# Performance work log

Hardware: AMD Instinct MI355X
Metric: run time of the kernel (lower is better)

Reference implementation:

```python
import jax, jax.numpy as jnp
import numpy as np
import math

HEAD_DIM = 128
DEPTH = 12
LAMBDA_INIT = 0.8 - 0.6 * math.exp(-0.3 * DEPTH)
EPS = 1e-5


def setup_inputs() -> dict:
    key = jax.random.key(0)
    ks = jax.random.split(key, 7)
    B, S, H2, D = 2, 2048, 16, HEAD_DIM  # H2 = 2 * num_diff_heads
    q = jax.random.normal(ks[0], (B, S, H2, D), dtype=jnp.float32)
    k = jax.random.normal(ks[1], (B, S, H2, D), dtype=jnp.float32)
    v = jax.random.normal(ks[2], (B, S, H2, D), dtype=jnp.float32)
    lambda_q1 = 0.1 * jax.random.normal(ks[3], (D,), dtype=jnp.float32)
    lambda_k1 = 0.1 * jax.random.normal(ks[4], (D,), dtype=jnp.float32)
    lambda_q2 = 0.1 * jax.random.normal(ks[5], (D,), dtype=jnp.float32)
    lambda_k2 = 0.1 * jax.random.normal(ks[6], (D,), dtype=jnp.float32)
    return {"q": q, "k": k, "v": v, "lambda_q1": lambda_q1, "lambda_k1": lambda_k1,
            "lambda_q2": lambda_q2, "lambda_k2": lambda_k2}


def _attn(qh, kh, v12, scale, causal_bias):
    # qh,kh: [B,S,H,D]; v12: [B,S,H,2D] (concat of v1,v2 -> same softmax shared,
    # identical math to the two separate flash calls attnX1/attnX2 concatenated)
    scores = jnp.einsum('bshd,bthd->bhst', qh, kh) * scale + causal_bias
    p = jax.nn.softmax(scores, axis=-1)
    return jnp.einsum('bhst,bthd->bshd', p, v12)  # [B,S,H,2D]


def reference(q, k, v, lambda_q1, lambda_k1, lambda_q2, lambda_k2):
    B, S, H2, D = q.shape
    H = H2 // 2
    scale = 1.0 / math.sqrt(D)
    # split_heads: '(H two) D' -> pairs of adjacent heads
    def split(x):
        x = x.reshape(B, S, H, 2, D)
        return x[..., 0, :], x[..., 1, :]
    q1, q2 = split(q)
    k1, k2 = split(k)
    v1, v2 = split(v)
    v12 = jnp.concatenate([v1, v2], axis=-1)  # [B,S,H,2D]

    causal_bias = jnp.where(jnp.tril(jnp.ones((S, S), dtype=bool)), 0.0,
                            jnp.float32(-jnp.inf))  # [S,S]

    attn1 = _attn(q1, k1, v12, scale, causal_bias)  # = cat(attn11, attn12)
    attn2 = _attn(q2, k2, v12, scale, causal_bias)  # = cat(attn21, attn22)

    lambda_1 = jnp.exp(jnp.sum(lambda_q1 * lambda_k1))
    lambda_2 = jnp.exp(jnp.sum(lambda_q2 * lambda_k2))
    lambda_full = lambda_1 - lambda_2 + LAMBDA_INIT

    attn = attn1 - lambda_full * attn2  # [B,S,H,2D]
    # RMSNorm over last dim (2D), no affine
    attn = attn * jax.lax.rsqrt(jnp.mean(attn * attn, axis=-1, keepdims=True) + EPS)
    attn = attn * (1.0 - LAMBDA_INIT)
    # '... H (two D) -> ... (H two) D'
    return attn.reshape(B, S, H, 2, D).reshape(B, S, H2, D)
```

## Files before the change

kernel.cpp:

```cpp
#include <hip/hip_runtime.h>
#include <math.h>


#define S_LEN 2048
#define ROWSTR 2048
#define NEG_BIG (-3.0e38f)
#define QSCALE (1.44269504088896f * 0.0883883476483184f)
#define SM_SHIFT 20.0f
#define LAMBDA_INIT 0.783605766532f

typedef __attribute__((ext_vector_type(8))) short short8;
typedef __attribute__((ext_vector_type(4))) float f32x4;

__device__ __forceinline__ short f2bf(float f) {
    unsigned u = __builtin_bit_cast(unsigned, f);
    u += 0x7fffu + ((u >> 16) & 1u);
    return (short)(u >> 16);
}

__device__ __forceinline__ void async16(const short* g, short* l) {
    __builtin_amdgcn_global_load_lds(
        (const __attribute__((address_space(1))) unsigned int*)g,
        (__attribute__((address_space(3))) unsigned int*)l, 16, 0, 0);
}

__global__ __launch_bounds__(256)
void prep_kernel(const float* __restrict__ k, const float* __restrict__ v,
                 short* __restrict__ kws, short* __restrict__ vws) {
    __shared__ short sT[32][258];
    const int tid = threadIdx.x;
    const int bh  = blockIdx.x >> 6;
    const int t   = blockIdx.x & 63;
    const int b   = bh >> 3;
    const int h   = bh & 7;

    {
        const int attn = tid >> 7;
        const int key  = (tid >> 2) & 31;
        const int tt   = tid & 3;
        const int s    = t * 32 + key;
        const float* src = k + (((size_t)(b * S_LEN + s) * 16) + 2 * h + attn) * 128 + tt * 32;
        short* kdst = kws + (((size_t)(bh * 64 + t)) << 13) + attn * 4096 + key * 128;
        #pragma unroll
        for (int i = 0; i < 4; ++i) {
            const int c = tt * 4 + i;
            float4 a0 = *(const float4*)(src + i * 8);
            float4 a1 = *(const float4*)(src + i * 8 + 4);
            short8 sv;
            sv[0]=f2bf(a0.x); sv[1]=f2bf(a0.y); sv[2]=f2bf(a0.z); sv[3]=f2bf(a0.w);
            sv[4]=f2bf(a1.x); sv[5]=f2bf(a1.y); sv[6]=f2bf(a1.z); sv[7]=f2bf(a1.w);
            *(short8*)(kdst + ((c ^ (key & 7)) << 3)) = sv;
        }
    }

    {
        const int key  = tid >> 3;
        const int part = tid & 7;
        const float* vsrc = v + (((size_t)(b * S_LEN + t * 32 + key) * 16) + 2 * h) * 128 + part * 32;
        #pragma unroll
        for (int i = 0; i < 4; ++i) {
            float4 a0 = *(const float4*)(vsrc + i * 8);
            float4 a1 = *(const float4*)(vsrc + i * 8 + 4);
            short8 sv;
            sv[0]=f2bf(a0.x); sv[1]=f2bf(a0.y); sv[2]=f2bf(a0.z); sv[3]=f2bf(a0.w);
            sv[4]=f2bf(a1.x); sv[5]=f2bf(a1.y); sv[6]=f2bf(a1.z); sv[7]=f2bf(a1.w);
            *(short8*)(&sT[key][part * 32 + i * 8]) = sv;
        }
    }
    __syncthreads();

    {
        short vv[32];
        #pragma unroll
        for (int key = 0; key < 32; ++key)
            vv[key] = sT[key][tid];
        short* vdst = vws + (((size_t)(bh * 64 + t)) << 13) + tid * 32;
        #pragma unroll
        for (int i = 0; i < 4; ++i)
            *(short8*)(vdst + i * 8) = *(short8*)&vv[i * 8];
    }
}

__global__ __launch_bounds__(256, 2)
void fda_kernel(const float* __restrict__ q,
                const short* __restrict__ kws, const short* __restrict__ vws,
                const float* __restrict__ lq1, const float* __restrict__ lk1,
                const float* __restrict__ lq2, const float* __restrict__ lk2,
                float* __restrict__ out) {
    __shared__ short sK[2][2][32][128];
    __shared__ short sV[2][256][32];
    __shared__ short sP[2][64][40];
    __shared__ float sL[2][64];
    __shared__ float sRed[2][2][32];

    const int tid  = threadIdx.x;
    const int w    = tid >> 6;
    const int lane = tid & 63;
    const int mi   = lane & 15;
    const int quad = lane >> 4;
    const int rg   = w & 1;
    const int u    = w >> 1;

    const int bid = blockIdx.x;
    const int bh  = bid & 15;
    const int g   = bid >> 4;
    const int qt  = (g < 16) ? (31 - g) : (g - 16);
    const int b   = bh >> 3;
    const int h   = bh & 7;
    const int qbase = qt * 64;
    const int nt  = 2 * qt + 2;

    const short* ktile0 = kws + (((size_t)(bh * 64)) << 13);
    const short* vtile0 = vws + (((size_t)(bh * 64)) << 13);

    {
        short* dk = &sK[0][0][0][0];
        short* dv = &sV[0][0][0];
        #pragma unroll
        for (int i = 0; i < 4; ++i) {
            const int ch = (w * 4 + i) * 512;
            async16(ktile0 + ch + lane * 8, dk + ch);
            async16(vtile0 + ch + lane * 8, dv + ch);
        }
    }

    float d1 = lq1[lane] * lk1[lane] + lq1[lane + 64] * lk1[lane + 64];
    float d2 = lq2[lane] * lk2[lane] + lq2[lane + 64] * lk2[lane + 64];
    #pragma unroll
    for (int off = 32; off; off >>= 1) {
        d1 += __shfl_xor(d1, off);
        d2 += __shfl_xor(d2, off);
    }
    const float lambda_full = expf(d1) - expf(d2) + LAMBDA_INIT;

    short8 qf[2][4];
    {
        #pragma unroll
        for (int m = 0; m < 2; ++m) {
            const int row = qbase + rg * 32 + m * 16 + mi;
            const float* qr = q + (((size_t)(b * S_LEN + row) * 16) + 2 * h + u) * 128 + quad * 8;
            #pragma unroll
            for (int db = 0; db < 4; ++db) {
                float4 a0 = *(const float4*)(qr + db * 32);
                float4 a1 = *(const float4*)(qr + db * 32 + 4);
                short8 sv;
                sv[0]=f2bf(a0.x*QSCALE); sv[1]=f2bf(a0.y*QSCALE); sv[2]=f2bf(a0.z*QSCALE); sv[3]=f2bf(a0.w*QSCALE);
                sv[4]=f2bf(a1.x*QSCALE); sv[5]=f2bf(a1.y*QSCALE); sv[6]=f2bf(a1.z*QSCALE); sv[7]=f2bf(a1.w*QSCALE);
                qf[m][db] = sv;
            }
        }
    }

    float l[2][4] = {{0.f,0.f,0.f,0.f},{0.f,0.f,0.f,0.f}};
    f32x4 O[2][2][8];
    #pragma unroll
    for (int a = 0; a < 2; ++a)
        #pragma unroll
        for (int m = 0; m < 2; ++m)
            #pragma unroll
            for (int nb = 0; nb < 8; ++nb)
                O[a][m][nb] = (f32x4){0.f, 0.f, 0.f, 0.f};

    for (int t = 0; t < nt; ++t) {
        __syncthreads();
        const int buf = t & 1;
        const bool act = (t <= 2 * qt + rg);

        if (act) {
            f32x4 S[2][2];
            #pragma unroll
            for (int m = 0; m < 2; ++m)
                #pragma unroll
                for (int kh = 0; kh < 2; ++kh)
                    S[m][kh] = (f32x4){0.f, 0.f, 0.f, 0.f};
            const short* kb = &sK[buf][u][0][0];
            #pragma unroll
            for (int db = 0; db < 4; ++db) {
                #pragma unroll
                for (int kh = 0; kh < 2; ++kh) {
                    const short8 kf = *(const short8*)(kb + (kh * 16 + mi) * 128 +
                                       ((((db << 2) + quad) ^ (mi & 7)) << 3));
                    S[0][kh] = __builtin_amdgcn_mfma_f32_16x16x32_bf16(qf[0][db], kf, S[0][kh], 0, 0, 0);
                    S[1][kh] = __builtin_amdgcn_mfma_f32_16x16x32_bf16(qf[1][db], kf, S[1][kh], 0, 0, 0);
                }
            }
            if (t == 2 * qt + rg) {
                const int qr0 = qbase + rg * 32;
                #pragma unroll
                for (int m = 0; m < 2; ++m)
                    #pragma unroll
                    for (int kh = 0; kh < 2; ++kh)
                        #pragma unroll
                        for (int r = 0; r < 4; ++r)
                            if (t * 32 + kh * 16 + mi > qr0 + m * 16 + quad * 4 + r)
                                S[m][kh][r] = NEG_BIG;
            }
            #pragma unroll
            for (int m = 0; m < 2; ++m) {
                short* pp = &sP[u][rg * 32 + m * 16 + quad * 4][mi];
                #pragma unroll
                for (int r = 0; r < 4; ++r) {
                    const float pa = exp2f(S[m][0][r] - SM_SHIFT);
                    const float pb = exp2f(S[m][1][r] - SM_SHIFT);
                    l[m][r] += pa + pb;
                    pp[r * 40]      = f2bf(pa);
                    pp[r * 40 + 16] = f2bf(pb);
                }
            }
        }
        __syncthreads();

        if (t + 1 < nt) {
            const short* kt = ktile0 + (((size_t)(t + 1)) << 13);
            const short* vt = vtile0 + (((size_t)(t + 1)) << 13);
            short* dk = &sK[buf ^ 1][0][0][0];
            short* dv = &sV[buf ^ 1][0][0];
            #pragma unroll
            for (int i = 0; i < 4; ++i) {
                const int ch = (w * 4 + i) * 512;
                async16(kt + ch + lane * 8, dk + ch);
                async16(vt + ch + lane * 8, dv + ch);
            }
        }

        if (act) {
            short8 pA[2][2];
            #pragma unroll
            for (int a = 0; a < 2; ++a)
                #pragma unroll
                for (int m = 0; m < 2; ++m)
                    pA[a][m] = *(const short8*)&sP[a][rg * 32 + m * 16 + mi][quad * 8];
            #pragma unroll
            for (int nb = 0; nb < 8; ++nb) {
                const short8 bv = *(const short8*)&sV[buf][u * 128 + nb * 16 + mi][quad * 8];
                O[0][0][nb] = __builtin_amdgcn_mfma_f32_16x16x32_bf16(pA[0][0], bv, O[0][0][nb], 0, 0, 0);
                O[0][1][nb] = __builtin_amdgcn_mfma_f32_16x16x32_bf16(pA[0][1], bv, O[0][1][nb], 0, 0, 0);
                O[1][0][nb] = __builtin_amdgcn_mfma_f32_16x16x32_bf16(pA[1][0], bv, O[1][0][nb], 0, 0, 0);
                O[1][1][nb] = __builtin_amdgcn_mfma_f32_16x16x32_bf16(pA[1][1], bv, O[1][1][nb], 0, 0, 0);
            }
        }
    }

    #pragma unroll
    for (int m = 0; m < 2; ++m)
        #pragma unroll
        for (int r = 0; r < 4; ++r) {
            float s = l[m][r];
            s += __shfl_xor(s, 1); s += __shfl_xor(s, 2);
            s += __shfl_xor(s, 4); s += __shfl_xor(s, 8);
            l[m][r] = s;
        }
    if (mi == 0) {
        #pragma unroll
        for (int m = 0; m < 2; ++m)
            #pragma unroll
            for (int r = 0; r < 4; ++r)
                sL[u][rg * 32 + m * 16 + quad * 4 + r] = l[m][r];
    }
    __syncthreads();

    float ss[2][4] = {{0.f,0.f,0.f,0.f},{0.f,0.f,0.f,0.f}};
    #pragma unroll
    for (int m = 0; m < 2; ++m)
        #pragma unroll
        for (int r = 0; r < 4; ++r) {
            const int row = rg * 32 + m * 16 + quad * 4 + r;
            const float il1 = 1.0f / sL[0][row];
            const float il2 = lambda_full / sL[1][row];
            #pragma unroll
            for (int nb = 0; nb < 8; ++nb) {
                const float c = O[0][m][nb][r] * il1 - O[1][m][nb][r] * il2;
                O[0][m][nb][r] = c;
                ss[m][r] += c * c;
            }
        }
    #pragma unroll
    for (int m = 0; m < 2; ++m)
        #pragma unroll
        for (int r = 0; r < 4; ++r) {
            float s = ss[m][r];
            s += __shfl_xor(s, 1); s += __shfl_xor(s, 2);
            s += __shfl_xor(s, 4); s += __shfl_xor(s, 8);
            ss[m][r] = s;
        }
    if (mi == 0) {
        #pragma unroll
        for (int m = 0; m < 2; ++m)
            #pragma unroll
            for (int r = 0; r < 4; ++r)
                sRed[rg][u][m * 16 + quad * 4 + r] = ss[m][r];
    }
    __syncthreads();

    #pragma unroll
    for (int m = 0; m < 2; ++m)
        #pragma unroll
        for (int r = 0; r < 4; ++r) {
            const int rl  = m * 16 + quad * 4 + r;
            const float tot = ss[m][r] + sRed[rg][u ^ 1][rl];
            const float scale = rsqrtf(tot * (1.0f / 256.0f) + 1e-5f) * (1.0f - LAMBDA_INIT);
            const int gr = qbase + rg * 32 + rl;
            float* ob = out + ((size_t)(b * S_LEN + gr)) * ROWSTR + h * 256 + u * 128 + mi;
            #pragma unroll
            for (int nb = 0; nb < 8; ++nb)
                ob[nb * 16] = O[0][m][nb][r] * scale;
        }
}

extern "C" void kernel_launch(void* const* d_in, const int* in_sizes, int n_in,
                              void* d_out, int out_size, void* d_ws, size_t ws_size,
                              hipStream_t stream) {
    (void)in_sizes; (void)n_in; (void)out_size; (void)ws_size;
    const float* q   = (const float*)d_in[0];
    const float* k   = (const float*)d_in[1];
    const float* v   = (const float*)d_in[2];
    const float* lq1 = (const float*)d_in[3];
    const float* lk1 = (const float*)d_in[4];
    const float* lq2 = (const float*)d_in[5];
    const float* lk2 = (const float*)d_in[6];
    float* out = (float*)d_out;

    short* kws = (short*)d_ws;
    short* vws = kws + (size_t)16 * 64 * 8192;

    prep_kernel<<<dim3(1024), dim3(256), 0, stream>>>(k, v, kws, vws);
    fda_kernel<<<dim3(512), dim3(256), 0, stream>>>(q, kws, vws,
                                                    lq1, lk1, lq2, lk2, out);
}
```

Before: 252.7 us.

## Coalesce prep loads via LDS staging, swizzle V tiles, prefetch earlier, add setprio

The prep kernel now stages K through shared memory with coalesced float4 loads and writes whole contiguous tiles out. V is written into a row-XOR-swizzled transpose buffer, and the attention kernel's V fragment reads use the matching swizzle to cut LDS bank conflicts. The next K/V tile prefetch is issued at the top of each iteration instead of after the softmax barrier, giving more overlap, and s_setprio brackets raise wave priority around the MFMA loops. The earlier prefetch relies on the double buffer being free at that point, and prep now uses more LDS.

```diff
diff --git a/kernel.cpp b/kernel.cpp
--- a/kernel.cpp
+++ b/kernel.cpp
@@ -27,7 +27,8 @@
 __global__ __launch_bounds__(256)
 void prep_kernel(const float* __restrict__ k, const float* __restrict__ v,
                  short* __restrict__ kws, short* __restrict__ vws) {
-    __shared__ short sT[32][258];
+    __shared__ short sKL[8192];
+    __shared__ short sT[32][260];
     const int tid = threadIdx.x;
     const int bh  = blockIdx.x >> 6;
     const int t   = blockIdx.x & 63;
@@ -35,45 +36,53 @@
     const int h   = bh & 7;
 
     {
-        const int attn = tid >> 7;
-        const int key  = (tid >> 2) & 31;
-        const int tt   = tid & 3;
-        const int s    = t * 32 + key;
-        const float* src = k + (((size_t)(b * S_LEN + s) * 16) + 2 * h + attn) * 128 + tt * 32;
-        short* kdst = kws + (((size_t)(bh * 64 + t)) << 13) + attn * 4096 + key * 128;
+        const int lh    = tid & 31;
+        const int c     = lh >> 1;
+        const int half  = lh & 1;
+        const int rbase = tid >> 5;
+        #pragma unroll
+        for (int p = 0; p < 8; ++p) {
+            const int row  = p * 8 + rbase;
+            const int attn = row >> 5;
+            const int key  = row & 31;
+            const float* src = k + (((size_t)(b * S_LEN + t * 32 + key) * 16) + 2 * h + attn) * 128 + lh * 4;
+            const float4 a = *(const float4*)src;
+            short4 sv;
+            sv.x = f2bf(a.x); sv.y = f2bf(a.y); sv.z = f2bf(a.z); sv.w = f2bf(a.w);
+            *(short4*)(sKL + attn * 4096 + key * 128 + ((c ^ (key & 7)) << 3) + half * 4) = sv;
+        }
+    }
+
+    {
+        const int n0 = (tid & 63) * 4;
+        const int kb = tid >> 6;
+        #pragma unroll
+        for (int p = 0; p < 8; ++p) {
+            const int key = p * 4 + kb;
+            const float* src = v + (((size_t)(b * S_LEN + t * 32 + key) * 16) + 2 * h) * 128 + n0;
+            const float4 a = *(const float4*)src;
+            short4 sv;
+            sv.x = f2bf(a.x); sv.y = f2bf(a.y); sv.z = f2bf(a.z); sv.w = f2bf(a.w);
+            *(short4*)(&sT[key][n0]) = sv;
+        }
+    }
+    __syncthreads();
+
+    {
+        short* kdst = kws + (((size_t)(bh * 64 + t)) << 13);
         #pragma unroll
         for (int i = 0; i < 4; ++i) {
-            const int c = tt * 4 + i;
-            float4 a0 = *(const float4*)(src + i * 8);
-            float4 a1 = *(const float4*)(src + i * 8 + 4);
-            short8 sv;
-            sv[0]=f2bf(a0.x); sv[1]=f2bf(a0.y); sv[2]=f2bf(a0.z); sv[3]=f2bf(a0.w);
-            sv[4]=f2bf(a1.x); sv[5]=f2bf(a1.y); sv[6]=f2bf(a1.z); sv[7]=f2bf(a1.w);
-            *(short8*)(kdst + ((c ^ (key & 7)) << 3)) = sv;
-        }
-    }
-
-    {
-        const int key  = tid >> 3;
-        const int part = tid & 7;
-        const float* vsrc = v + (((size_t)(b * S_LEN + t * 32 + key) * 16) + 2 * h) * 128 + part * 32;
-        #pragma unroll
-        for (int i = 0; i < 4; ++i) {
-            float4 a0 = *(const float4*)(vsrc + i * 8);
-            float4 a1 = *(const float4*)(vsrc + i * 8 + 4);
-            short8 sv;
-            sv[0]=f2bf(a0.x); sv[1]=f2bf(a0.y); sv[2]=f2bf(a0.z); sv[3]=f2bf(a0.w);
-            sv[4]=f2bf(a1.x); sv[5]=f2bf(a1.y); sv[6]=f2bf(a1.z); sv[7]=f2bf(a1.w);
-            *(short8*)(&sT[key][part * 32 + i * 8]) = sv;
-        }
-    }
-    __syncthreads();
-
-    {
+            const short8 d = *(const short8*)(sKL + i * 2048 + tid * 8);
+            *(short8*)(kdst + i * 2048 + tid * 8) = d;
+        }
+    }
+
+    {
+        const int f = (tid >> 1) & 3;
         short vv[32];
         #pragma unroll
-        for (int key = 0; key < 32; ++key)
-            vv[key] = sT[key][tid];
+        for (int o = 0; o < 32; ++o)
+            vv[o] = sT[(((o >> 3) ^ f) << 3) + (o & 7)][tid];
         short* vdst = vws + (((size_t)(bh * 64 + t)) << 13) + tid * 32;
         #pragma unroll
         for (int i = 0; i < 4; ++i)
@@ -82,8 +91,8 @@
 }
 
 __global__ __launch_bounds__(256, 2)
-void fda_kernel(const float* __restrict__ q,
-                const short* __restrict__ kws, const short* __restrict__ vws,
+void fda_kernel(const short* __restrict__ kws, const short* __restrict__ vws,
+                const float* __restrict__ q,
                 const float* __restrict__ lq1, const float* __restrict__ lk1,
                 const float* __restrict__ lq2, const float* __restrict__ lk2,
                 float* __restrict__ out) {
@@ -134,20 +143,18 @@
     const float lambda_full = expf(d1) - expf(d2) + LAMBDA_INIT;
 
     short8 qf[2][4];
-    {
-        #pragma unroll
-        for (int m = 0; m < 2; ++m) {
-            const int row = qbase + rg * 32 + m * 16 + mi;
-            const float* qr = q + (((size_t)(b * S_LEN + row) * 16) + 2 * h + u) * 128 + quad * 8;
-            #pragma unroll
-            for (int db = 0; db < 4; ++db) {
-                float4 a0 = *(const float4*)(qr + db * 32);
-                float4 a1 = *(const float4*)(qr + db * 32 + 4);
-                short8 sv;
-                sv[0]=f2bf(a0.x*QSCALE); sv[1]=f2bf(a0.y*QSCALE); sv[2]=f2bf(a0.z*QSCALE); sv[3]=f2bf(a0.w*QSCALE);
-                sv[4]=f2bf(a1.x*QSCALE); sv[5]=f2bf(a1.y*QSCALE); sv[6]=f2bf(a1.z*QSCALE); sv[7]=f2bf(a1.w*QSCALE);
-                qf[m][db] = sv;
-            }
+    #pragma unroll
+    for (int m = 0; m < 2; ++m) {
+        const int row = qbase + rg * 32 + m * 16 + mi;
+        const float* qr = q + (((size_t)(b * S_LEN + row) * 16) + 2 * h + u) * 128 + quad * 8;
+        #pragma unroll
+        for (int db = 0; db < 4; ++db) {
+            float4 a0 = *(const float4*)(qr + db * 32);
+            float4 a1 = *(const float4*)(qr + db * 32 + 4);
+            short8 sv;
+            sv[0]=f2bf(a0.x*QSCALE); sv[1]=f2bf(a0.y*QSCALE); sv[2]=f2bf(a0.z*QSCALE); sv[3]=f2bf(a0.w*QSCALE);
+            sv[4]=f2bf(a1.x*QSCALE); sv[5]=f2bf(a1.y*QSCALE); sv[6]=f2bf(a1.z*QSCALE); sv[7]=f2bf(a1.w*QSCALE);
+            qf[m][db] = sv;
         }
     }
 
@@ -160,12 +167,27 @@
             #pragma unroll
             for (int nb = 0; nb < 8; ++nb)
                 O[a][m][nb] = (f32x4){0.f, 0.f, 0.f, 0.f};
+
+    const int vswz = (quad ^ ((mi >> 1) & 3)) << 3;
 
     for (int t = 0; t < nt; ++t) {
         __syncthreads();
         const int buf = t & 1;
+
+        if (t + 1 < nt) {
+            const short* kt = ktile0 + (((size_t)(t + 1)) << 13);
+            const short* vt = vtile0 + (((size_t)(t + 1)) << 13);
+            short* dk = &sK[buf ^ 1][0][0][0];
+            short* dv = &sV[buf ^ 1][0][0];
+            #pragma unroll
+            for (int i = 0; i < 4; ++i) {
+                const int ch = (w * 4 + i) * 512;
+                async16(kt + ch + lane * 8, dk + ch);
+                async16(vt + ch + lane * 8, dv + ch);
+            }
+        }
+
         const bool act = (t <= 2 * qt + rg);
-
         if (act) {
             f32x4 S[2][2];
             #pragma unroll
@@ -174,6 +196,7 @@
                 for (int kh = 0; kh < 2; ++kh)
                     S[m][kh] = (f32x4){0.f, 0.f, 0.f, 0.f};
             const short* kb = &sK[buf][u][0][0];
+            __builtin_amdgcn_s_setprio(1);
             #pragma unroll
             for (int db = 0; db < 4; ++db) {
                 #pragma unroll
@@ -184,6 +207,7 @@
                     S[1][kh] = __builtin_amdgcn_mfma_f32_16x16x32_bf16(qf[1][db], kf, S[1][kh], 0, 0, 0);
                 }
             }
+            __builtin_amdgcn_s_setprio(0);
             if (t == 2 * qt + rg) {
                 const int qr0 = qbase + rg * 32;
                 #pragma unroll
@@ -210,19 +234,6 @@
         }
         __syncthreads();
 
-        if (t + 1 < nt) {
-            const short* kt = ktile0 + (((size_t)(t + 1)) << 13);
-            const short* vt = vtile0 + (((size_t)(t + 1)) << 13);
-            short* dk = &sK[buf ^ 1][0][0][0];
-            short* dv = &sV[buf ^ 1][0][0];
-            #pragma unroll
-            for (int i = 0; i < 4; ++i) {
-                const int ch = (w * 4 + i) * 512;
-                async16(kt + ch + lane * 8, dk + ch);
-                async16(vt + ch + lane * 8, dv + ch);
-            }
-        }
-
         if (act) {
             short8 pA[2][2];
             #pragma unroll
@@ -230,14 +241,16 @@
                 #pragma unroll
                 for (int m = 0; m < 2; ++m)
                     pA[a][m] = *(const short8*)&sP[a][rg * 32 + m * 16 + mi][quad * 8];
+            __builtin_amdgcn_s_setprio(1);
             #pragma unroll
             for (int nb = 0; nb < 8; ++nb) {
-                const short8 bv = *(const short8*)&sV[buf][u * 128 + nb * 16 + mi][quad * 8];
+                const short8 bv = *(const short8*)&sV[buf][u * 128 + nb * 16 + mi][vswz];
                 O[0][0][nb] = __builtin_amdgcn_mfma_f32_16x16x32_bf16(pA[0][0], bv, O[0][0][nb], 0, 0, 0);
                 O[0][1][nb] = __builtin_amdgcn_mfma_f32_16x16x32_bf16(pA[0][1], bv, O[0][1][nb], 0, 0, 0);
                 O[1][0][nb] = __builtin_amdgcn_mfma_f32_16x16x32_bf16(pA[1][0], bv, O[1][0][nb], 0, 0, 0);
                 O[1][1][nb] = __builtin_amdgcn_mfma_f32_16x16x32_bf16(pA[1][1], bv, O[1][1][nb], 0, 0, 0);
             }
+            __builtin_amdgcn_s_setprio(0);
         }
     }
 
@@ -324,6 +337,6 @@
     short* vws = kws + (size_t)16 * 64 * 8192;
 
     prep_kernel<<<dim3(1024), dim3(256), 0, stream>>>(k, v, kws, vws);
-    fda_kernel<<<dim3(512), dim3(256), 0, stream>>>(q, kws, vws,
+    fda_kernel<<<dim3(512), dim3(256), 0, stream>>>(kws, vws, q,
                                                     lq1, lk1, lq2, lk2, out);
 }
```

New measurement: 245.9 us. 2.7% less time.
